# Kernel optimization log

Hardware: AMD Instinct MI355X
Metric: run time of the kernel (lower is better)

The kernel has to match this reference:

```python
import jax, jax.numpy as jnp
import numpy as np
from jax import lax

C = 128; G = 8; K = 3; P = K * K; GC = C // G
N, H, W = 4, 96, 96
EPS = 1e-5

def conv_bn_silu(x, w, gamma, beta, rmean, rvar, stride, pad):
    # Conv2d(bias=False) + BatchNorm2d(eval) + SiLU, NCHW
    y = lax.conv_general_dilated(x, w, (stride, stride), [(pad, pad), (pad, pad)],
                                 dimension_numbers=('NCHW', 'OIHW', 'NCHW'))
    s = gamma / jnp.sqrt(rvar + EPS)
    y = y * s[None, :, None, None] + (beta - rmean * s)[None, :, None, None]
    return y * jax.nn.sigmoid(y)

def dcnv3(x, dw_w, dw_b, ln_g, ln_b, off_w, off_b, m_w, m_b, ip_w, ip_b, op_w, op_b):
    # InternImage DCNv3, channels-last input (N,H,W,C), k=3 s=1 pad=1 dil=1 group=G, offset_scale=1
    n, h, w, c = x.shape
    xp = x @ ip_w.T + ip_b  # input_proj
    # offset/mask branch: depthwise 3x3 conv + LayerNorm + GELU on the ORIGINAL input
    dw = lax.conv_general_dilated(x, dw_w, (1, 1), [(1, 1), (1, 1)],
                                  dimension_numbers=('NHWC', 'HWIO', 'NHWC'),
                                  feature_group_count=c) + dw_b
    dw = (dw - dw.mean(-1, keepdims=True)) / jnp.sqrt(dw.var(-1, keepdims=True) + EPS) * ln_g + ln_b
    dw = jax.nn.gelu(dw)
    off = (dw @ off_w.T + off_b).reshape(n, h, w, G, P, 2)  # (..., (dx, dy))
    m = jax.nn.softmax((dw @ m_w.T + m_b).reshape(n, h, w, G, P), -1)
    pad = 1
    hp, wp = h + 2 * pad, w + 2 * pad
    xpad = jnp.pad(xp, ((0, 0), (pad, pad), (pad, pad), (0, 0))).reshape(n, hp, wp, G, GC)
    ky, kx = jnp.meshgrid(jnp.arange(-1, 2, dtype=x.dtype), jnp.arange(-1, 2, dtype=x.dtype), indexing='ij')
    # absolute sampling coords in padded image (grid_sample align_corners=False equivalent)
    py = (jnp.arange(h, dtype=x.dtype) + pad)[None, :, None, None, None] + ky.reshape(-1) + off[..., 1]
    px = (jnp.arange(w, dtype=x.dtype) + pad)[None, None, :, None, None] + kx.reshape(-1) + off[..., 0]
    yf = jnp.floor(py); xf = jnp.floor(px)
    wy = py - yf; wx = px - xf
    y0 = yf.astype(jnp.int32); x0 = xf.astype(jnp.int32)
    n_idx = jnp.arange(n)[:, None, None, None, None]
    g_idx = jnp.arange(G)[None, None, None, :, None]

    def gat(yi, xi):
        valid = ((yi >= 0) & (yi < hp) & (xi >= 0) & (xi < wp)).astype(x.dtype)
        v = xpad[n_idx, jnp.clip(yi, 0, hp - 1), jnp.clip(xi, 0, wp - 1), g_idx]  # (n,h,w,G,P,GC)
        return v * valid[..., None]

    v = (gat(y0, x0) * ((1 - wy) * (1 - wx))[..., None]
         + gat(y0, x0 + 1) * ((1 - wy) * wx)[..., None]
         + gat(y0 + 1, x0) * (wy * (1 - wx))[..., None]
         + gat(y0 + 1, x0 + 1) * (wy * wx)[..., None])
    out = jnp.einsum('nhwgpc,nhwgp->nhwgc', v, m).reshape(n, h, w, c)
    return out @ op_w.T + op_b  # output_proj

def _forward(x0, x1, x2, conv_w, conv_g, conv_b, conv_rm, conv_rv,
             conv1_w, conv1_g, conv1_b, conv1_rm, conv1_rv,
             conv2_w, conv2_g, conv2_b, conv2_rm, conv2_rv,
             dw_w, dw_b, ln_g, ln_b, off_w, off_b, m_w, m_b, ip_w, ip_b, op_w, op_b):
    n, _, h, w = x0.shape
    # x1: 256 ch > 128 -> self.conv (1x1); smaller spatial -> bilinear upsample to HW
    y1 = conv_bn_silu(x1, conv_w, conv_g, conv_b, conv_rm, conv_rv, 1, 0)
    feat_up1 = jax.image.resize(y1, (n, C, h, w), method='bilinear')
    # x2: 64 ch < 128 -> self.conv1 (1x1); larger spatial -> self.conv2 (3x3 s2) to HW
    y2 = conv_bn_silu(x2, conv1_w, conv1_g, conv1_b, conv1_rm, conv1_rv, 1, 0)
    feat_up2 = conv_bn_silu(y2, conv2_w, conv2_g, conv2_b, conv2_rm, conv2_rv, 2, 1)
    d1 = dcnv3(feat_up1.transpose(0, 2, 3, 1), dw_w, dw_b, ln_g, ln_b, off_w, off_b, m_w, m_b, ip_w, ip_b, op_w, op_b)
    d2 = dcnv3(feat_up2.transpose(0, 2, 3, 1), dw_w, dw_b, ln_g, ln_b, off_w, off_b, m_w, m_b, ip_w, ip_b, op_w, op_b)
    a1 = jax.nn.relu(d1).transpose(0, 3, 1, 2)
    a2 = jax.nn.relu(d2).transpose(0, 3, 1, 2)
    return jnp.concatenate([a1, x0, a2], axis=1)  # (N, 3C, H, W)

def setup_inputs():
    ks = jax.random.split(jax.random.key(0), 24)
    f = jnp.float32
    return {
        'x0': jax.random.normal(ks[0], (N, C, H, W), f),
        'x1': jax.random.normal(ks[1], (N, 2 * C, H // 2, W // 2), f),
        'x2': jax.random.normal(ks[2], (N, C // 2, 2 * H, 2 * W), f),
        'conv_w': jax.random.normal(ks[3], (C, 2 * C, 1, 1), f) * 0.05,
        'conv_g': jnp.ones((C,), f), 'conv_b': jnp.zeros((C,), f),
        'conv_rm': jax.random.normal(ks[4], (C,), f) * 0.1,
        'conv_rv': jax.random.uniform(ks[5], (C,), f) + 0.5,
        'conv1_w': jax.random.normal(ks[6], (C, C // 2, 1, 1), f) * 0.08,
        'conv1_g': jnp.ones((C,), f), 'conv1_b': jnp.zeros((C,), f),
        'conv1_rm': jax.random.normal(ks[7], (C,), f) * 0.1,
        'conv1_rv': jax.random.uniform(ks[8], (C,), f) + 0.5,
        'conv2_w': jax.random.normal(ks[9], (C, C, 3, 3), f) * 0.03,
        'conv2_g': jnp.ones((C,), f), 'conv2_b': jnp.zeros((C,), f),
        'conv2_rm': jax.random.normal(ks[10], (C,), f) * 0.1,
        'conv2_rv': jax.random.uniform(ks[11], (C,), f) + 0.5,
        'dw_w': jax.random.normal(ks[12], (3, 3, 1, C), f) * 0.1,
        'dw_b': jnp.zeros((C,), f),
        'ln_g': jnp.ones((C,), f), 'ln_b': jnp.zeros((C,), f),
        'off_w': jax.random.normal(ks[13], (G * P * 2, C), f) * 0.01,
        'off_b': jnp.zeros((G * P * 2,), f),
        'm_w': jax.random.normal(ks[14], (G * P, C), f) * 0.05,
        'm_b': jnp.zeros((G * P,), f),
        'ip_w': jax.random.normal(ks[15], (C, C), f) * 0.05,
        'ip_b': jnp.zeros((C,), f),
        'op_w': jax.random.normal(ks[16], (C, C), f) * 0.05,
        'op_b': jnp.zeros((C,), f),
    }

def reference(x0, x1, x2, conv_w, conv_g, conv_b, conv_rm, conv_rv,
              conv1_w, conv1_g, conv1_b, conv1_rm, conv1_rv,
              conv2_w, conv2_g, conv2_b, conv2_rm, conv2_rv,
              dw_w, dw_b, ln_g, ln_b, off_w, off_b, m_w, m_b, ip_w, ip_b, op_w, op_b):
    return _forward(x0, x1, x2, conv_w, conv_g, conv_b, conv_rm, conv_rv,
                    conv1_w, conv1_g, conv1_b, conv1_rm, conv1_rv,
                    conv2_w, conv2_g, conv2_b, conv2_rm, conv2_rv,
                    dw_w, dw_b, ln_g, ln_b, off_w, off_b, m_w, m_b, ip_w, ip_b, op_w, op_b)
```

## Files before the change

kernel.cpp:

```cpp
#include <hip/hip_runtime.h>
#include <cstdint>
#include <cstddef>

#define EPSV 1e-5f
#define NPIX 9216
#define LDA 136
#define LDK 72

typedef __bf16 bf16;
typedef _Float16 f16;
typedef __attribute__((ext_vector_type(8))) __bf16 bf16x8;
typedef __attribute__((ext_vector_type(4))) __bf16 bf16x4;
typedef __attribute__((ext_vector_type(2))) _Float16 f16x2;
typedef __attribute__((ext_vector_type(4))) float  f32x4;

__device__ __forceinline__ float silu_f(float v) { return v / (1.f + __expf(-v)); }

__global__ __launch_bounds__(256) void prep_kernel(
    const float* __restrict__ conv_w, const float* __restrict__ conv_g,
    const float* __restrict__ conv_b, const float* __restrict__ conv_rm, const float* __restrict__ conv_rv,
    const float* __restrict__ conv1_w, const float* __restrict__ conv1_g,
    const float* __restrict__ conv1_b, const float* __restrict__ conv1_rm, const float* __restrict__ conv1_rv,
    const float* __restrict__ conv2_w, const float* __restrict__ conv2_g,
    const float* __restrict__ conv2_bb, const float* __restrict__ conv2_rm, const float* __restrict__ conv2_rv,
    const float* __restrict__ ip_w, const float* __restrict__ op_w,
    const float* __restrict__ off_w, const float* __restrict__ m_w,
    const float* __restrict__ off_b, const float* __restrict__ m_b,
    float* __restrict__ WTSf, bf16* __restrict__ WTSb)
{
  int idx = blockIdx.x * 256 + threadIdx.x;
  if (idx < 608) {
    if (idx < 128) {
      int co = idx;
      float s = conv_g[co] * rsqrtf(conv_rv[co] + EPSV);
      WTSf[idx] = conv_b[co] - conv_rm[co] * s;
    } else if (idx < 256) {
      int co = idx - 128;
      float s = conv1_g[co] * rsqrtf(conv1_rv[co] + EPSV);
      WTSf[idx] = conv1_b[co] - conv1_rm[co] * s;
    } else if (idx < 384) {
      int co = idx - 256;
      float s = conv2_g[co] * rsqrtf(conv2_rv[co] + EPSV);
      WTSf[idx] = conv2_bb[co] - conv2_rm[co] * s;
    } else {
      int col = idx - 384;
      WTSf[idx] = (col < 144) ? off_b[col] : (col < 216 ? m_b[col - 144] : 0.f);
    }
  } else {
    int j = idx - 608;
    if (j < 32768) {
      int co = j >> 8, ci = j & 255;
      float s = conv_g[co] * rsqrtf(conv_rv[co] + EPSV);
      WTSb[j] = (bf16)(conv_w[co * 256 + ci] * s);
    } else if (j < 40960) {
      int r = j - 32768; int co = r >> 6, ci = r & 63;
      float s = conv1_g[co] * rsqrtf(conv1_rv[co] + EPSV);
      WTSb[j] = (bf16)(conv1_w[co * 64 + ci] * s);
    } else if (j < 188416) {
      int r = j - 40960; int kp = r >> 14; int rr = r & 16383;
      int co = rr >> 7, ci = rr & 127;
      float s = conv2_g[co] * rsqrtf(conv2_rv[co] + EPSV);
      WTSb[j] = (bf16)(conv2_w[(co * 128 + ci) * 9 + kp] * s);
    } else if (j < 204800) {
      int r = j - 188416; int co = r >> 7, ci = r & 127;
      WTSb[j] = (bf16)ip_w[co * 128 + ci];
    } else if (j < 233472) {
      int r = j - 204800; int co = r >> 7, ci = r & 127;
      float v = (co < 144) ? off_w[co * 128 + ci] : (co < 216 ? m_w[(co - 144) * 128 + ci] : 0.f);
      WTSb[j] = (bf16)v;
    } else if (j < 249856) {
      int r = j - 233472; int co = r >> 7, ci = r & 127;
      WTSb[j] = (bf16)op_w[co * 128 + ci];
    }
  }
}

__global__ __launch_bounds__(256) void c1x1_mfma_kernel(
    const float* __restrict__ x, const bf16* __restrict__ W,
    const float* __restrict__ bias, int K, int HW, bf16* __restrict__ outb)
{
  __shared__ bf16 As[64 * LDK];
  __shared__ bf16 Bs[128 * LDK];
  int m0 = blockIdx.x << 6;
  int t = threadIdx.x;
  int n = m0 / HW; int hw0 = m0 - n * HW;
  const float* xn = x + (size_t)n * K * HW;
  int wv = t >> 6, lane = t & 63;
  int lrow = lane & 15, q = lane >> 4;
  int n0 = wv * 32;
  f32x4 acc[4][2];
#pragma unroll
  for (int i = 0; i < 4; ++i)
#pragma unroll
    for (int j = 0; j < 2; ++j)
#pragma unroll
      for (int e = 0; e < 4; ++e) acc[i][j][e] = 0.f;

  for (int k0 = 0; k0 < K; k0 += 64) {
    if (k0) __syncthreads();
    for (int i = t; i < 1024; i += 256) {
      int px = i & 63; int ci4 = (i >> 6) << 2;
      bf16x4 p;
#pragma unroll
      for (int j = 0; j < 4; ++j)
        p[j] = (bf16)xn[(size_t)(k0 + ci4 + j) * HW + hw0 + px];
      *(bf16x4*)&As[px * LDK + ci4] = p;
    }
    for (int i = t; i < 1024; i += 256) {
      int co = i >> 3; int k8 = (i & 7) << 3;
      *(bf16x8*)&Bs[co * LDK + k8] = *(const bf16x8*)&W[(size_t)co * K + k0 + k8];
    }
    __syncthreads();
#pragma unroll
    for (int ks = 0; ks < 2; ++ks) {
      int ko = ks * 32 + q * 8;
      bf16x8 bfr0 = *(const bf16x8*)&Bs[(n0 + lrow) * LDK + ko];
      bf16x8 bfr1 = *(const bf16x8*)&Bs[(n0 + 16 + lrow) * LDK + ko];
#pragma unroll
      for (int mi = 0; mi < 4; ++mi) {
        bf16x8 afr = *(const bf16x8*)&As[(mi * 16 + lrow) * LDK + ko];
        acc[mi][0] = __builtin_amdgcn_mfma_f32_16x16x32_bf16(afr, bfr0, acc[mi][0], 0, 0, 0);
        acc[mi][1] = __builtin_amdgcn_mfma_f32_16x16x32_bf16(afr, bfr1, acc[mi][1], 0, 0, 0);
      }
    }
  }
#pragma unroll
  for (int mi = 0; mi < 4; ++mi) {
#pragma unroll
    for (int nj = 0; nj < 2; ++nj) {
      int co = n0 + nj * 16 + lrow;
      float bb = bias[co];
#pragma unroll
      for (int r = 0; r < 4; ++r) {
        int m = m0 + mi * 16 + q * 4 + r;
        outb[(size_t)m * 128 + co] = (bf16)silu_f(acc[mi][nj][r] + bb);
      }
    }
  }
}

__global__ __launch_bounds__(256) void upsample_kernel(
    const bf16* __restrict__ y1b, bf16* __restrict__ feat1b)
{
  int idx = blockIdx.x * 256 + threadIdx.x;
  int c4 = (idx & 31) << 2;
  int pw = idx >> 5;
  int ow = pw % 96; int t1 = pw / 96;
  int oh = t1 % 96; int n = t1 / 96;
  float sh = oh * 0.5f - 0.25f, sw = ow * 0.5f - 0.25f;
  float hf = floorf(sh), wf = floorf(sw);
  float fy = sh - hf, fx = sw - wf;
  int h0 = (int)hf, w0 = (int)wf;
  int h0c = max(h0, 0), h1c = min(h0 + 1, 47);
  int w0c = max(w0, 0), w1c = min(w0 + 1, 47);
  const bf16* yn = y1b + (size_t)n * 2304 * 128 + c4;
  bf16x4 v00 = *(const bf16x4*)&yn[(h0c * 48 + w0c) * 128];
  bf16x4 v01 = *(const bf16x4*)&yn[(h0c * 48 + w1c) * 128];
  bf16x4 v10 = *(const bf16x4*)&yn[(h1c * 48 + w0c) * 128];
  bf16x4 v11 = *(const bf16x4*)&yn[(h1c * 48 + w1c) * 128];
  bf16x4 o;
#pragma unroll
  for (int e = 0; e < 4; ++e) {
    float v = (1.f - fy) * ((1.f - fx) * (float)v00[e] + fx * (float)v01[e])
            + fy * ((1.f - fx) * (float)v10[e] + fx * (float)v11[e]);
    o[e] = (bf16)v;
  }
  *(bf16x4*)&feat1b[((size_t)n * NPIX + oh * 96 + ow) * 128 + c4] = o;
}

__global__ __launch_bounds__(256) void conv2_mfma_kernel(
    const bf16* __restrict__ y2b, const bf16* __restrict__ W2b,
    const float* __restrict__ b2, bf16* __restrict__ feat2b)
{
  __shared__ bf16 As[64 * LDA];
  __shared__ bf16 Bs[128 * LDA];
  int m0 = blockIdx.x << 6;
  int t = threadIdx.x;
  int wv = t >> 6, lane = t & 63;
  int lrow = lane & 15, q = lane >> 4;
  int n0 = wv * 32;
  f32x4 acc[4][2];
#pragma unroll
  for (int i = 0; i < 4; ++i)
#pragma unroll
    for (int j = 0; j < 2; ++j)
#pragma unroll
      for (int e = 0; e < 4; ++e) acc[i][j][e] = 0.f;
  bf16x8 zv;
#pragma unroll
  for (int e = 0; e < 8; ++e) zv[e] = (bf16)0.f;

  for (int kp = 0; kp < 9; ++kp) {
    int kh = kp / 3, kw = kp - kh * 3;
    __syncthreads();
    for (int i = t; i < 1024; i += 256) {
      int row = i >> 4; int c8 = (i & 15) << 3;
      int m = m0 + row;
      int nimg = m / NPIX; int hw = m - nimg * NPIX;
      int oh = hw / 96, ow = hw - oh * 96;
      int ih = 2 * oh - 1 + kh, iw = 2 * ow - 1 + kw;
      bf16x8 v = zv;
      if ((unsigned)ih < 192u && (unsigned)iw < 192u)
        v = *(const bf16x8*)&y2b[(((size_t)nimg * 192 + ih) * 192 + iw) * 128 + c8];
      *(bf16x8*)&As[row * LDA + c8] = v;
    }
    const bf16* Wk = W2b + kp * 16384;
    for (int i = t; i < 2048; i += 256) {
      int nn = i >> 4; int k8 = (i & 15) << 3;
      *(bf16x8*)&Bs[nn * LDA + k8] = *(const bf16x8*)&Wk[nn * 128 + k8];
    }
    __syncthreads();
#pragma unroll
    for (int ks = 0; ks < 4; ++ks) {
      bf16x8 bfr0 = *(const bf16x8*)&Bs[(n0 + lrow) * LDA + ks * 32 + q * 8];
      bf16x8 bfr1 = *(const bf16x8*)&Bs[(n0 + 16 + lrow) * LDA + ks * 32 + q * 8];
#pragma unroll
      for (int mi = 0; mi < 4; ++mi) {
        bf16x8 afr = *(const bf16x8*)&As[(mi * 16 + lrow) * LDA + ks * 32 + q * 8];
        acc[mi][0] = __builtin_amdgcn_mfma_f32_16x16x32_bf16(afr, bfr0, acc[mi][0], 0, 0, 0);
        acc[mi][1] = __builtin_amdgcn_mfma_f32_16x16x32_bf16(afr, bfr1, acc[mi][1], 0, 0, 0);
      }
    }
  }
#pragma unroll
  for (int mi = 0; mi < 4; ++mi) {
#pragma unroll
    for (int nj = 0; nj < 2; ++nj) {
      int co = n0 + nj * 16 + lrow;
      float bb = b2[co];
#pragma unroll
      for (int r = 0; r < 4; ++r) {
        int m = m0 + mi * 16 + q * 4 + r;
        feat2b[(size_t)m * 128 + co] = (bf16)silu_f(acc[mi][nj][r] + bb);
      }
    }
  }
}

__global__ __launch_bounds__(256) void mm_bf16_kernel(
    const bf16* __restrict__ A, const bf16* __restrict__ W,
    const float* __restrict__ bias, int Nc, int ostride, int act,
    int store_mode, void* __restrict__ outp)
{
  __shared__ bf16 As[64 * LDA];
  __shared__ bf16 Bs[128 * LDA];
  int m0 = blockIdx.x << 6;
  int nb = blockIdx.y << 7;
  int cols_here = Nc - nb; if (cols_here > 128) cols_here = 128;
  int t = threadIdx.x;
  for (int i = t; i < 1024; i += 256) {
    int row = i >> 4; int c8 = (i & 15) << 3;
    *(bf16x8*)&As[row * LDA + c8] = *(const bf16x8*)&A[(size_t)(m0 + row) * 128 + c8];
  }
  bf16x8 zv;
#pragma unroll
  for (int e = 0; e < 8; ++e) zv[e] = (bf16)0.f;
  for (int i = t; i < 2048; i += 256) {
    int n = i >> 4; int k8 = (i & 15) << 3;
    bf16x8 v = (n < cols_here) ? *(const bf16x8*)&W[(size_t)(nb + n) * 128 + k8] : zv;
    *(bf16x8*)&Bs[n * LDA + k8] = v;
  }
  __syncthreads();

  int wv = t >> 6, lane = t & 63;
  int lrow = lane & 15, q = lane >> 4;
  int n0 = wv * 32;
  f32x4 acc[4][2];
#pragma unroll
  for (int i = 0; i < 4; ++i)
#pragma unroll
    for (int j = 0; j < 2; ++j)
#pragma unroll
      for (int e = 0; e < 4; ++e) acc[i][j][e] = 0.f;

#pragma unroll
  for (int ks = 0; ks < 4; ++ks) {
    bf16x8 bfr0 = *(const bf16x8*)&Bs[(n0 + lrow) * LDA + ks * 32 + q * 8];
    bf16x8 bfr1 = *(const bf16x8*)&Bs[(n0 + 16 + lrow) * LDA + ks * 32 + q * 8];
#pragma unroll
    for (int mi = 0; mi < 4; ++mi) {
      bf16x8 afr = *(const bf16x8*)&As[(mi * 16 + lrow) * LDA + ks * 32 + q * 8];
      acc[mi][0] = __builtin_amdgcn_mfma_f32_16x16x32_bf16(afr, bfr0, acc[mi][0], 0, 0, 0);
      acc[mi][1] = __builtin_amdgcn_mfma_f32_16x16x32_bf16(afr, bfr1, acc[mi][1], 0, 0, 0);
    }
  }

  float* outf = (float*)outp;
  bf16*  outb = (bf16*)outp;
  f16*   outh = (f16*)outp;
#pragma unroll
  for (int mi = 0; mi < 4; ++mi) {
#pragma unroll
    for (int nj = 0; nj < 2; ++nj) {
      int col = nb + n0 + nj * 16 + lrow;
      if (col >= Nc) continue;
      float bb = bias[col];
#pragma unroll
      for (int r = 0; r < 4; ++r) {
        int m = m0 + mi * 16 + q * 4 + r;
        float v = acc[mi][nj][r] + bb;
        if (act == 1) v = fmaxf(v, 0.f);
        if (store_mode == 0) {
          outf[(size_t)m * ostride + col] = v;
        } else if (store_mode == 2) {
          outb[(size_t)m * 128 + col] = (bf16)v;
        } else if (store_mode == 3) {
          outh[(size_t)m * ostride + col] = (f16)v;
        } else {
          int nn = m / NPIX; int hw = m - nn * NPIX;
          int img = nn & 3; int choff = (nn >= 4) ? 256 : 0;
          outf[((size_t)(img * 384 + choff + col)) * NPIX + hw] = v;
        }
      }
    }
  }
}

__global__ __launch_bounds__(256) void dwln_kernel(
    const bf16* __restrict__ featb, const float* __restrict__ dw_w,
    const float* __restrict__ dw_b, const float* __restrict__ ln_g,
    const float* __restrict__ ln_b, bf16* __restrict__ dwgb)
{
  int t = threadIdx.x;
  int pxl = t >> 4;
  int c8 = (t & 15) << 3;
  int pixel = blockIdx.x * 16 + pxl;
  int n = pixel / NPIX; int hw = pixel - n * NPIX;
  int h = hw / 96; int w = hw - h * 96;
  const bf16* fn = featb + (size_t)n * NPIX * 128 + c8;
  float acc[8];
#pragma unroll
  for (int e = 0; e < 8; ++e) acc[e] = dw_b[c8 + e];
#pragma unroll
  for (int kh = 0; kh < 3; ++kh) {
    int hh = h + kh - 1;
    if ((unsigned)hh >= 96u) continue;
#pragma unroll
    for (int kw = 0; kw < 3; ++kw) {
      int ww = w + kw - 1;
      if ((unsigned)ww >= 96u) continue;
      bf16x8 v = *(const bf16x8*)&fn[(hh * 96 + ww) * 128];
      const float* wt = &dw_w[(kh * 3 + kw) * 128 + c8];
#pragma unroll
      for (int e = 0; e < 8; ++e) acc[e] += (float)v[e] * wt[e];
    }
  }
  float s = 0.f, qs = 0.f;
#pragma unroll
  for (int e = 0; e < 8; ++e) { s += acc[e]; qs += acc[e] * acc[e]; }
#pragma unroll
  for (int off = 8; off > 0; off >>= 1) {
    s  += __shfl_xor(s, off);
    qs += __shfl_xor(qs, off);
  }
  float mean = s * (1.f / 128.f);
  float var = qs * (1.f / 128.f) - mean * mean;
  float rstd = rsqrtf(var + EPSV);
  bf16x8 o;
#pragma unroll
  for (int e = 0; e < 8; ++e) {
    float xn = (acc[e] - mean) * rstd * ln_g[c8 + e] + ln_b[c8 + e];
    float z = 0.7978845608028654f * (xn + 0.044715f * xn * xn * xn);
    float th;
    if (z > 15.f) th = 1.f;
    else if (z < -15.f) th = -1.f;
    else { float e2 = __expf(2.f * z); th = (e2 - 1.f) / (e2 + 1.f); }
    o[e] = (bf16)(0.5f * xn * (1.f + th));
  }
  *(bf16x8*)&dwgb[(size_t)pixel * 128 + c8] = o;
}

__global__ __launch_bounds__(256) void sample_kernel(
    const bf16* __restrict__ xpb, const f16* __restrict__ offm,
    bf16* __restrict__ vaggb)
{
  __shared__ uint32_t Sd[16 * 112];
  const f16* S = (const f16*)Sd;
  int t = threadIdx.x;
  int bid = blockIdx.x;
  int wg = (bid & 7) * 576 + (bid >> 3);
  {
    const uint32_t* src = (const uint32_t*)(offm + (size_t)wg * 16 * 224);
    for (int i = t; i < 1792; i += 256) Sd[i] = src[i];
  }
  __syncthreads();
  int pxl = t >> 4;
  int tid16 = t & 15;
  int g = tid16 >> 1;
  int c8 = (tid16 & 1) << 3;
  int pixel = wg * 16 + pxl;
  int n = pixel / NPIX; int hw = pixel - n * NPIX;
  int h = hw / 96; int w = hw - h * 96;
  const f16* Sp = S + pxl * 224;
  float lg[9]; float mx = -1e30f;
#pragma unroll
  for (int p = 0; p < 9; ++p) { lg[p] = (float)Sp[144 + g * 9 + p]; mx = fmaxf(mx, lg[p]); }
  float se = 0.f;
#pragma unroll
  for (int p = 0; p < 9; ++p) { lg[p] = __expf(lg[p] - mx); se += lg[p]; }
  float inv = 1.f / se;
  const bf16* xpn = xpb + (size_t)n * NPIX * 128 + g * 16 + c8;
  float acc[8];
#pragma unroll
  for (int e = 0; e < 8; ++e) acc[e] = 0.f;
#pragma unroll
  for (int p = 0; p < 9; ++p) {
    f16x2 d2 = *(const f16x2*)&Sp[g * 18 + p * 2];
    float dx = (float)d2.x, dy = (float)d2.y;
    float pyu = (float)(h + p / 3 - 1) + dy;
    float pxu = (float)(w + p % 3 - 1) + dx;
    float yf = floorf(pyu), xf = floorf(pxu);
    float wy = pyu - yf, wx = pxu - xf;
    int y0 = (int)yf, x0 = (int)xf;
    float ay0 = ((unsigned)y0 < 96u) ? (1.f - wy) : 0.f;
    float ay1 = ((unsigned)(y0 + 1) < 96u) ? wy : 0.f;
    float ax0 = ((unsigned)x0 < 96u) ? (1.f - wx) : 0.f;
    float ax1 = ((unsigned)(x0 + 1) < 96u) ? wx : 0.f;
    int y0c = min(max(y0, 0), 95), y1c = min(max(y0 + 1, 0), 95);
    int x0c = min(max(x0, 0), 95), x1c = min(max(x0 + 1, 0), 95);
    float mp = lg[p] * inv;
    float w00 = ay0 * ax0 * mp, w01 = ay0 * ax1 * mp;
    float w10 = ay1 * ax0 * mp, w11 = ay1 * ax1 * mp;
    bf16x8 v00 = *(const bf16x8*)&xpn[(y0c * 96 + x0c) * 128];
    bf16x8 v01 = *(const bf16x8*)&xpn[(y0c * 96 + x1c) * 128];
    bf16x8 v10 = *(const bf16x8*)&xpn[(y1c * 96 + x0c) * 128];
    bf16x8 v11 = *(const bf16x8*)&xpn[(y1c * 96 + x1c) * 128];
#pragma unroll
    for (int e = 0; e < 8; ++e) {
      acc[e] += w00 * (float)v00[e] + w01 * (float)v01[e]
              + w10 * (float)v10[e] + w11 * (float)v11[e];
    }
  }
  bf16x8 o;
#pragma unroll
  for (int e = 0; e < 8; ++e) o[e] = (bf16)acc[e];
  *(bf16x8*)&vaggb[(size_t)pixel * 128 + g * 16 + c8] = o;
}

__global__ __launch_bounds__(256) void copy_x0_kernel(
    const float4* __restrict__ x0, float4* __restrict__ out)
{
  int idx = blockIdx.x * 256 + threadIdx.x;
  int n = idx / (128 * 2304);
  int r = idx - n * (128 * 2304);
  out[(size_t)(n * 384 + 128) * 2304 + r] = x0[(size_t)n * 128 * 2304 + r];
}

extern "C" void kernel_launch(void* const* d_in, const int* in_sizes, int n_in,
                              void* d_out, int out_size, void* d_ws, size_t ws_size,
                              hipStream_t stream)
{
  (void)in_sizes; (void)n_in; (void)out_size; (void)ws_size;
  const float* x0      = (const float*)d_in[0];
  const float* x1      = (const float*)d_in[1];
  const float* x2      = (const float*)d_in[2];
  const float* conv_w  = (const float*)d_in[3];
  const float* conv_g  = (const float*)d_in[4];
  const float* conv_b  = (const float*)d_in[5];
  const float* conv_rm = (const float*)d_in[6];
  const float* conv_rv = (const float*)d_in[7];
  const float* conv1_w = (const float*)d_in[8];
  const float* conv1_g = (const float*)d_in[9];
  const float* conv1_b = (const float*)d_in[10];
  const float* conv1_rm= (const float*)d_in[11];
  const float* conv1_rv= (const float*)d_in[12];
  const float* conv2_w = (const float*)d_in[13];
  const float* conv2_g = (const float*)d_in[14];
  const float* conv2_b = (const float*)d_in[15];
  const float* conv2_rm= (const float*)d_in[16];
  const float* conv2_rv= (const float*)d_in[17];
  const float* dw_w    = (const float*)d_in[18];
  const float* dw_b    = (const float*)d_in[19];
  const float* ln_g    = (const float*)d_in[20];
  const float* ln_b    = (const float*)d_in[21];
  const float* off_w   = (const float*)d_in[22];
  const float* off_b   = (const float*)d_in[23];
  const float* m_w     = (const float*)d_in[24];
  const float* m_b     = (const float*)d_in[25];
  const float* ip_w    = (const float*)d_in[26];
  const float* ip_b    = (const float*)d_in[27];
  const float* op_w    = (const float*)d_in[28];
  const float* op_b    = (const float*)d_in[29];
  float* out = (float*)d_out;
  char* WS = (char*)d_ws;

  bf16* featb  = (bf16*)WS;
  bf16* feat1b = featb;
  bf16* feat2b = featb + 4718592;
  bf16* y2b    = (bf16*)(WS + 18874368);
  bf16* xpb    = (bf16*)(WS + 18874368);
  bf16* dwgb   = (bf16*)(WS + 37748736);
  bf16* vaggb  = dwgb;
  bf16* y1b    = (bf16*)(WS + 56623104);
  f16*  offm   = (f16*)(WS + 58982400);
  float* WTSf  = (float*)(WS + 125042688);
  bf16*  WTSb  = (bf16*)(WS + 125045120);

  float* b1f  = WTSf;
  float* b1bf = WTSf + 128;
  float* b2f  = WTSf + 256;
  float* bomf = WTSf + 384;
  bf16* W1b  = WTSb;
  bf16* W1bb = WTSb + 32768;
  bf16* W2b  = WTSb + 40960;
  bf16* Wipb = WTSb + 188416;
  bf16* Womb = WTSb + 204800;
  bf16* Wopb = WTSb + 233472;

  prep_kernel<<<979, 256, 0, stream>>>(
      conv_w, conv_g, conv_b, conv_rm, conv_rv,
      conv1_w, conv1_g, conv1_b, conv1_rm, conv1_rv,
      conv2_w, conv2_g, conv2_b, conv2_rm, conv2_rv,
      ip_w, op_w, off_w, m_w, off_b, m_b, WTSf, WTSb);

  c1x1_mfma_kernel<<<144, 256, 0, stream>>>(x1, W1b, b1f, 256, 2304, y1b);
  upsample_kernel<<<4608, 256, 0, stream>>>(y1b, feat1b);

  c1x1_mfma_kernel<<<2304, 256, 0, stream>>>(x2, W1bb, b1bf, 64, 36864, y2b);
  conv2_mfma_kernel<<<576, 256, 0, stream>>>(y2b, W2b, b2f, feat2b);

  mm_bf16_kernel<<<dim3(1152, 1), 256, 0, stream>>>(featb, Wipb, ip_b, 128, 128, 0, 2, xpb);
  dwln_kernel<<<4608, 256, 0, stream>>>(featb, dw_w, dw_b, ln_g, ln_b, dwgb);
  mm_bf16_kernel<<<dim3(1152, 2), 256, 0, stream>>>(dwgb, Womb, bomf, 224, 224, 0, 3, offm);
  sample_kernel<<<4608, 256, 0, stream>>>(xpb, offm, vaggb);
  mm_bf16_kernel<<<dim3(1152, 1), 256, 0, stream>>>(vaggb, Wopb, op_b, 128, 0, 1, 1, out);

  copy_x0_kernel<<<4608, 256, 0, stream>>>((const float4*)x0, (float4*)out);
}
```

Baseline: 421.0 us.

## Share softmax via LDS, cap sample kernel registers, remap dwln block order

The sample kernel now computes the per-(pixel,group) mask softmax once in shared memory with 128 threads, instead of redundantly in every channel-half thread. It partially unrolls the tap loop (outer loop not unrolled) and sets a minimum of 6 blocks per SM to reduce register pressure and raise occupancy for the latency-bound gathers. The dwln kernel adopts the same interleaved block-to-tile mapping as the sample kernel. The cost is an extra barrier and some LDS usage, and the tighter register limit could cause spills.

```diff
diff --git a/kernel.cpp b/kernel.cpp
--- a/kernel.cpp
+++ b/kernel.cpp
@@ -324,7 +324,9 @@
   int t = threadIdx.x;
   int pxl = t >> 4;
   int c8 = (t & 15) << 3;
-  int pixel = blockIdx.x * 16 + pxl;
+  int bid = blockIdx.x;
+  int wg = (bid & 7) * 576 + (bid >> 3);
+  int pixel = wg * 16 + pxl;
   int n = pixel / NPIX; int hw = pixel - n * NPIX;
   int h = hw / 96; int w = hw - h * 96;
   const bf16* fn = featb + (size_t)n * NPIX * 128 + c8;
@@ -370,11 +372,12 @@
   *(bf16x8*)&dwgb[(size_t)pixel * 128 + c8] = o;
 }
 
-__global__ __launch_bounds__(256) void sample_kernel(
+__global__ __launch_bounds__(256, 6) void sample_kernel(
     const bf16* __restrict__ xpb, const f16* __restrict__ offm,
     bf16* __restrict__ vaggb)
 {
   __shared__ uint32_t Sd[16 * 112];
+  __shared__ float Pm[16 * 72];
   const f16* S = (const f16*)Sd;
   int t = threadIdx.x;
   int bid = blockIdx.x;
@@ -382,6 +385,21 @@
   {
     const uint32_t* src = (const uint32_t*)(offm + (size_t)wg * 16 * 224);
     for (int i = t; i < 1792; i += 256) Sd[i] = src[i];
+  }
+  __syncthreads();
+  if (t < 128) {
+    int px = t >> 3, gg = t & 7;
+    const f16* L = S + px * 224 + 144 + gg * 9;
+    float l[9]; float mx = -1e30f;
+#pragma unroll
+    for (int p = 0; p < 9; ++p) { l[p] = (float)L[p]; mx = fmaxf(mx, l[p]); }
+    float se = 0.f;
+#pragma unroll
+    for (int p = 0; p < 9; ++p) { l[p] = __expf(l[p] - mx); se += l[p]; }
+    float inv = 1.f / se;
+    float* Pp = Pm + px * 72 + gg * 9;
+#pragma unroll
+    for (int p = 0; p < 9; ++p) Pp[p] = l[p] * inv;
   }
   __syncthreads();
   int pxl = t >> 4;
@@ -391,44 +409,42 @@
   int pixel = wg * 16 + pxl;
   int n = pixel / NPIX; int hw = pixel - n * NPIX;
   int h = hw / 96; int w = hw - h * 96;
-  const f16* Sp = S + pxl * 224;
-  float lg[9]; float mx = -1e30f;
-#pragma unroll
-  for (int p = 0; p < 9; ++p) { lg[p] = (float)Sp[144 + g * 9 + p]; mx = fmaxf(mx, lg[p]); }
-  float se = 0.f;
-#pragma unroll
-  for (int p = 0; p < 9; ++p) { lg[p] = __expf(lg[p] - mx); se += lg[p]; }
-  float inv = 1.f / se;
+  const f16* Sp = S + pxl * 224 + g * 18;
+  const float* Pp = Pm + pxl * 72 + g * 9;
   const bf16* xpn = xpb + (size_t)n * NPIX * 128 + g * 16 + c8;
   float acc[8];
 #pragma unroll
   for (int e = 0; e < 8; ++e) acc[e] = 0.f;
-#pragma unroll
-  for (int p = 0; p < 9; ++p) {
-    f16x2 d2 = *(const f16x2*)&Sp[g * 18 + p * 2];
-    float dx = (float)d2.x, dy = (float)d2.y;
-    float pyu = (float)(h + p / 3 - 1) + dy;
-    float pxu = (float)(w + p % 3 - 1) + dx;
-    float yf = floorf(pyu), xf = floorf(pxu);
-    float wy = pyu - yf, wx = pxu - xf;
-    int y0 = (int)yf, x0 = (int)xf;
-    float ay0 = ((unsigned)y0 < 96u) ? (1.f - wy) : 0.f;
-    float ay1 = ((unsigned)(y0 + 1) < 96u) ? wy : 0.f;
-    float ax0 = ((unsigned)x0 < 96u) ? (1.f - wx) : 0.f;
-    float ax1 = ((unsigned)(x0 + 1) < 96u) ? wx : 0.f;
-    int y0c = min(max(y0, 0), 95), y1c = min(max(y0 + 1, 0), 95);
-    int x0c = min(max(x0, 0), 95), x1c = min(max(x0 + 1, 0), 95);
-    float mp = lg[p] * inv;
-    float w00 = ay0 * ax0 * mp, w01 = ay0 * ax1 * mp;
-    float w10 = ay1 * ax0 * mp, w11 = ay1 * ax1 * mp;
-    bf16x8 v00 = *(const bf16x8*)&xpn[(y0c * 96 + x0c) * 128];
-    bf16x8 v01 = *(const bf16x8*)&xpn[(y0c * 96 + x1c) * 128];
-    bf16x8 v10 = *(const bf16x8*)&xpn[(y1c * 96 + x0c) * 128];
-    bf16x8 v11 = *(const bf16x8*)&xpn[(y1c * 96 + x1c) * 128];
-#pragma unroll
-    for (int e = 0; e < 8; ++e) {
-      acc[e] += w00 * (float)v00[e] + w01 * (float)v01[e]
-              + w10 * (float)v10[e] + w11 * (float)v11[e];
+#pragma unroll 1
+  for (int kh = 0; kh < 3; ++kh) {
+#pragma unroll
+    for (int kw = 0; kw < 3; ++kw) {
+      int p = kh * 3 + kw;
+      f16x2 d2 = *(const f16x2*)&Sp[p * 2];
+      float dx = (float)d2.x, dy = (float)d2.y;
+      float pyu = (float)(h + kh - 1) + dy;
+      float pxu = (float)(w + kw - 1) + dx;
+      float yf = floorf(pyu), xf = floorf(pxu);
+      float wy = pyu - yf, wx = pxu - xf;
+      int y0 = (int)yf, x0 = (int)xf;
+      float ay0 = ((unsigned)y0 < 96u) ? (1.f - wy) : 0.f;
+      float ay1 = ((unsigned)(y0 + 1) < 96u) ? wy : 0.f;
+      float ax0 = ((unsigned)x0 < 96u) ? (1.f - wx) : 0.f;
+      float ax1 = ((unsigned)(x0 + 1) < 96u) ? wx : 0.f;
+      int y0c = min(max(y0, 0), 95), y1c = min(max(y0 + 1, 0), 95);
+      int x0c = min(max(x0, 0), 95), x1c = min(max(x0 + 1, 0), 95);
+      float mp = Pp[p];
+      float w00 = ay0 * ax0 * mp, w01 = ay0 * ax1 * mp;
+      float w10 = ay1 * ax0 * mp, w11 = ay1 * ax1 * mp;
+      bf16x8 v00 = *(const bf16x8*)&xpn[(y0c * 96 + x0c) * 128];
+      bf16x8 v01 = *(const bf16x8*)&xpn[(y0c * 96 + x1c) * 128];
+      bf16x8 v10 = *(const bf16x8*)&xpn[(y1c * 96 + x0c) * 128];
+      bf16x8 v11 = *(const bf16x8*)&xpn[(y1c * 96 + x1c) * 128];
+#pragma unroll
+      for (int e = 0; e < 8; ++e) {
+        acc[e] += w00 * (float)v00[e] + w01 * (float)v01[e]
+                + w10 * (float)v10[e] + w11 * (float)v11[e];
+      }
     }
   }
   bf16x8 o;
```

New measurement: 429.5 us. 2.0% more time.
